# Optimization experiments

Hardware: AMD Instinct MI355X
Metric: run time of the kernel (lower is better)

Reference implementation:

```python
import jax, jax.numpy as jnp
import numpy as np

B, Himg, Wimg, C, HID, R = 16, 64, 64, 256, 512, 2
CLIP = 3.0
NULL_LOGIT = 0.0
WARMUP_ETA = 1.0


def _ln(x, g, b, eps=1e-5):
    m = x.mean(-1, keepdims=True)
    v = ((x - m) ** 2).mean(-1, keepdims=True)
    return (x - m) * jax.lax.rsqrt(v + eps) * g + b


def _mlp(x, W1, b1, W2, b2):
    # Linear -> GELU (erf, torch default) -> Linear
    return jax.nn.gelu(x @ W1 + b1, approximate=False) @ W2 + b2


def setup_inputs() -> dict:
    key = jax.random.key(0)
    ks = jax.random.split(key, 8)
    s = 0.02
    return {
        "states": jax.random.normal(ks[0], (B, Himg * Wimg, C), jnp.float32),
        "ln_c_g": jnp.ones((C,), jnp.float32),
        "ln_c_b": jnp.zeros((C,), jnp.float32),
        "parent_seed": jax.random.normal(ks[1], (1, 1, C), jnp.float32) * s,
        "dW1": jax.random.normal(ks[2], (3 * C, HID), jnp.float32) * s,
        "db1": jnp.zeros((HID,), jnp.float32),
        "dW2": jax.random.normal(ks[3], (HID, 1), jnp.float32) * s,
        "db2": jnp.zeros((1,), jnp.float32),
        "rW1": jax.random.normal(ks[4], (3 * C, HID), jnp.float32) * s,
        "rb1": jnp.zeros((HID,), jnp.float32),
        "rW2": jax.random.normal(ks[5], (HID, 1), jnp.float32) * s,
        "rb2": jnp.zeros((1,), jnp.float32),
        "vW": jax.random.normal(ks[6], (C, C), jnp.float32) * s,
        "vb": jnp.zeros((C,), jnp.float32),
        "e_bias": jnp.full((1,), -0.1, jnp.float32),
        "ln_o_g": jnp.ones((C,), jnp.float32),
        "ln_o_b": jnp.zeros((C,), jnp.float32),
        "image_h": Himg,
        "image_w": Wimg,
    }


def reference(states, ln_c_g, ln_c_b, parent_seed, dW1, db1, dW2, db2,
              rW1, rb1, rW2, rb2, vW, vb, e_bias, ln_o_g, ln_o_b,
              image_h, image_w):
    b = states.shape[0]
    ph, pw = image_h // R, image_w // R
    # [B,H,W,C] -> [B, ph*pw, R*R, C] local 2x2 child groups
    grid = states.reshape(b, image_h, image_w, C)
    groups = grid.reshape(b, ph, R, pw, R, C).transpose(0, 1, 3, 2, 4, 5)
    groups = groups.reshape(b, ph * pw, R * R, C)

    normalized = _ln(groups, ln_c_g, ln_c_b)            # child LayerNorm
    gm = normalized.mean(axis=2, keepdims=True)          # group mean (mask all-true)
    gm_b = jnp.broadcast_to(gm, normalized.shape)
    joint = jnp.concatenate([normalized, gm_b, normalized * gm_b], axis=-1)

    drive = _mlp(joint, dW1, db1, dW2, db2)              # [B,P,G,1]
    variance = ((normalized - gm) ** 2).mean(-1, keepdims=True)
    resistance = jax.nn.softplus(_mlp(joint, rW1, rb1, rW2, rb2)) + variance

    # EMLUnit: clipped drive/resistance energy with learned bias
    energy = jnp.clip(WARMUP_ETA * drive / (resistance + 1e-6) + e_bias,
                      -CLIP, CLIP)[..., 0]               # [B,P,G]

    # EMLResponsibility: null-aware softmax over children + null slot
    null = jnp.full(energy.shape[:-1] + (1,), NULL_LOGIT, energy.dtype)
    probs = jax.nn.softmax(jnp.concatenate([energy, null], axis=-1), axis=-1)
    weights = probs[..., :-1]                            # neighbor_weights [B,P,G]
    null_weight = probs[..., -1:]                        # [B,P,1]
    update_strength = 1.0 - null_weight                  # [B,P,1]

    values = normalized @ vW + vb                        # value_proj
    candidate = jnp.einsum('bpg,bpgc->bpc', weights, values)

    # EMLPrecisionUpdate with old_confidence=0: blend seed toward candidate
    old_state = parent_seed                              # broadcasts over [B,P,C]
    new_state = old_state + update_strength * (candidate - old_state)
    parent_state = _ln(new_state, ln_o_g, ln_o_b)
    return parent_state
```

## Files before the change

### kernel.cpp

```cpp
#include <hip/hip_runtime.h>
#include <hip/hip_bf16.h>
#include <math.h>

#define BATCH 16
#define PGRID 1024
#define NGRP  (BATCH*PGRID)
#define NELEM (NGRP*4)
#define CDIM  256
#define HID   512

#define OFF_NH    ((size_t)0)
#define OFF_NL    ((size_t)8388608)
#define OFF_GMH   ((size_t)16777216)
#define OFF_GML   ((size_t)18874368)
#define OFF_VAR   ((size_t)20971520)
#define OFF_DRIVE ((size_t)21037056)
#define OFF_RPRE  ((size_t)21102592)
#define OFF_WN    ((size_t)21168128)
#define OFF_US    ((size_t)25362432)
#define OFF_W1TH  ((size_t)25378816)
#define OFF_W1TL  ((size_t)25772032)

__device__ __forceinline__ unsigned short f2bf(float x) {
  unsigned u = __float_as_uint(x);
  unsigned r = u + 0x7FFFu + ((u >> 16) & 1u);
  return (unsigned short)(r >> 16);
}
__device__ __forceinline__ float bf2f(unsigned short h) {
  return __uint_as_float(((unsigned)h) << 16);
}

__device__ __forceinline__ void wave_reduce4(float v[4]) {
#pragma unroll
  for (int off = 1; off < 64; off <<= 1) {
#pragma unroll
    for (int i = 0; i < 4; ++i) v[i] += __shfl_xor(v[i], off, 64);
  }
}

__device__ __forceinline__ void block_reduce4(float v[4], float* sh ) {
  wave_reduce4(v);
  const int lane = threadIdx.x & 63, wid = threadIdx.x >> 6;
  __syncthreads();
  if (lane == 0) {
#pragma unroll
    for (int i = 0; i < 4; ++i) sh[wid * 4 + i] = v[i];
  }
  __syncthreads();
#pragma unroll
  for (int i = 0; i < 4; ++i) v[i] = sh[i] + sh[4 + i] + sh[8 + i] + sh[12 + i];
}

__global__ __launch_bounds__(256) void prep_kernel(
    const float* __restrict__ states,
    const float* __restrict__ ln_c_g, const float* __restrict__ ln_c_b,
    short* __restrict__ nh, short* __restrict__ nl,
    short* __restrict__ gmh, short* __restrict__ gml,
    float* __restrict__ varb, float* __restrict__ drive, float* __restrict__ rpre)
{
  __shared__ float sh[16];
  const int g = blockIdx.x;
  const int b = g >> 10;
  const int p = g & 1023;
  const int py = p >> 5, px = p & 31;
  const int c = threadIdx.x;

  float x[4];
#pragma unroll
  for (int s = 0; s < 4; ++s) {
    const int h = py * 2 + (s >> 1);
    const int w = px * 2 + (s & 1);
    x[s] = states[((size_t)(b * 4096 + h * 64 + w)) * CDIM + c];
  }

  float sum[4] = {x[0], x[1], x[2], x[3]};
  block_reduce4(sum, sh);
  float d[4];
#pragma unroll
  for (int s = 0; s < 4; ++s) d[s] = x[s] - sum[s] * (1.f / 256.f);

  float sq[4] = {d[0]*d[0], d[1]*d[1], d[2]*d[2], d[3]*d[3]};
  block_reduce4(sq, sh);

  const float gg = ln_c_g[c], bb = ln_c_b[c];
  float nn[4];
#pragma unroll
  for (int s = 0; s < 4; ++s)
    nn[s] = d[s] * rsqrtf(sq[s] * (1.f / 256.f) + 1e-5f) * gg + bb;

  const float gmc = 0.25f * (nn[0] + nn[1] + nn[2] + nn[3]);
  float e4[4];
#pragma unroll
  for (int s = 0; s < 4; ++s) { const float t = nn[s] - gmc; e4[s] = t * t; }
  block_reduce4(e4, sh);

  const size_t nb = (size_t)g * 4 * CDIM;
#pragma unroll
  for (int s = 0; s < 4; ++s) {
    const unsigned short h = f2bf(nn[s]);
    const unsigned short l = f2bf(nn[s] - bf2f(h));
    nh[nb + s * CDIM + c] = (short)h;
    nl[nb + s * CDIM + c] = (short)l;
  }
  {
    const unsigned short h = f2bf(gmc);
    const unsigned short l = f2bf(gmc - bf2f(h));
    gmh[(size_t)g * CDIM + c] = (short)h;
    gml[(size_t)g * CDIM + c] = (short)l;
  }
  if (c < 4) {
    varb[g * 4 + c] = e4[c] * (1.f / 256.f);
    drive[g * 4 + c] = 0.f;
    rpre[g * 4 + c] = 0.f;
  }
}

__global__ __launch_bounds__(256) void prew1_kernel(
    const float* __restrict__ dW1, const float* __restrict__ rW1,
    short* __restrict__ w1th, short* __restrict__ w1tl)
{
  const int col = blockIdx.x;
  const float* W1 = (col < 512) ? dW1 : rW1;
  const int cl = (col < 512) ? col : col - 512;
  for (int k = threadIdx.x; k < 768; k += 256) {
    const float x = W1[(size_t)k * HID + cl];
    const unsigned short h = f2bf(x);
    const unsigned short l = f2bf(x - bf2f(h));
    w1th[(size_t)col * 768 + k] = (short)h;
    w1tl[(size_t)col * 768 + k] = (short)l;
  }
}

typedef __attribute__((ext_vector_type(8))) short  frag_ab;
typedef __attribute__((ext_vector_type(4))) float  frag_cd;

#define AIDX(sec, row) ((sec) * 1024 + (row) * 8)

__global__ __launch_bounds__(256, 2) void mlp_gemm_mfma(
    const short* __restrict__ nh, const short* __restrict__ nl,
    const short* __restrict__ gmh, const short* __restrict__ gml,
    const short* __restrict__ w1th, const short* __restrict__ w1tl,
    const float* __restrict__ db1, const float* __restrict__ rb1,
    const float* __restrict__ dW2, const float* __restrict__ rW2,
    float* __restrict__ drive, float* __restrict__ rpre)
{
  __shared__ __align__(16) short Ah[8192];
  __shared__ __align__(16) short Al[8192];
  __shared__ __align__(16) short Bh[8192];
  __shared__ __align__(16) short Bl[8192];

  const int tid  = threadIdx.x;
  const int lane = tid & 63;
  const int w    = tid >> 6;
  const int wm   = w >> 1;
  const int wn   = w & 1;

  const int bid = blockIdx.x;
  const int xcd = bid & 7;
  const int lb  = bid >> 3;
  const int mt  = xcd * 64 + (lb >> 3);
  const int nt  = lb & 7;
  const int m_base = mt * 128;
  const int n_base = nt * 128;

  const int srow = tid & 127;
  const int sp   = tid >> 7;
  const int sp16 = sp * 16;
  const int sp2  = sp * 2;

  const short* nhrow = nh  + (size_t)(m_base + srow) * CDIM;
  const short* nlrow = nl  + (size_t)(m_base + srow) * CDIM;
  const short* ghrow = gmh + (size_t)((m_base + srow) >> 2) * CDIM;
  const short* glrow = gml + (size_t)((m_base + srow) >> 2) * CDIM;
  const short* bsrc_h = w1th + (size_t)(n_base + srow) * 768 + sp16;
  const short* bsrc_l = w1tl + (size_t)(n_base + srow) * 768 + sp16;

  frag_cd acc[4][4];
#pragma unroll
  for (int i = 0; i < 4; ++i)
#pragma unroll
    for (int j = 0; j < 4; ++j)
#pragma unroll
      for (int q = 0; q < 4; ++q) acc[i][j][q] = 0.f;

  frag_ab rA0, rA1, rA2, rA3, rA4, rA5, rA6, rA7;
  frag_ab sB0, sB1, sB2, sB3;

#define LOADA(K0) do {                                                   \
    const int k0_ = (K0);                                                \
    if (k0_ < 256) {                                                     \
      const short* p_ = nhrow + k0_ + sp16;                              \
      const short* q_ = nlrow + k0_ + sp16;                              \
      rA0 = *(const frag_ab*)(p_);  rA1 = *(const frag_ab*)(p_ + 8);     \
      rA2 = *(const frag_ab*)(q_);  rA3 = *(const frag_ab*)(q_ + 8);     \
    } else if (k0_ < 512) {                                              \
      const short* p_ = ghrow + (k0_ - 256) + sp16;                      \
      const short* q_ = glrow + (k0_ - 256) + sp16;                      \
      rA0 = *(const frag_ab*)(p_);  rA1 = *(const frag_ab*)(p_ + 8);     \
      rA2 = *(const frag_ab*)(q_);  rA3 = *(const frag_ab*)(q_ + 8);     \
    } else {                                                             \
      const int kb_ = k0_ - 512;                                         \
      const short* p_ = nhrow + kb_ + sp16;                              \
      const short* q_ = nlrow + kb_ + sp16;                              \
      const short* r_ = ghrow + kb_ + sp16;                              \
      const short* s_ = glrow + kb_ + sp16;                              \
      rA0 = *(const frag_ab*)(p_);  rA1 = *(const frag_ab*)(p_ + 8);     \
      rA2 = *(const frag_ab*)(q_);  rA3 = *(const frag_ab*)(q_ + 8);     \
      rA4 = *(const frag_ab*)(r_);  rA5 = *(const frag_ab*)(r_ + 8);     \
      rA6 = *(const frag_ab*)(s_);  rA7 = *(const frag_ab*)(s_ + 8);     \
    }                                                                    \
  } while (0)

#define LOADB(K0) do {                                                   \
    sB0 = *(const frag_ab*)(bsrc_h + (K0));                              \
    sB1 = *(const frag_ab*)(bsrc_h + (K0) + 8);                          \
    sB2 = *(const frag_ab*)(bsrc_l + (K0));                              \
    sB3 = *(const frag_ab*)(bsrc_l + (K0) + 8);                          \
  } while (0)

#define STOREAB(BUF, RAW) do {                                           \
    const int bo_ = (BUF) * 4096;                                        \
    if (RAW) {                                                           \
      *(frag_ab*)&Ah[bo_ + AIDX(sp2,     srow)] = rA0;                   \
      *(frag_ab*)&Ah[bo_ + AIDX(sp2 + 1, srow)] = rA1;                   \
      *(frag_ab*)&Al[bo_ + AIDX(sp2,     srow)] = rA2;                   \
      *(frag_ab*)&Al[bo_ + AIDX(sp2 + 1, srow)] = rA3;                   \
    } else {                                                             \
      frag_ab ph0, ph1, pl0, pl1;                                        \
      _Pragma("unroll")                                                  \
      for (int j_ = 0; j_ < 8; ++j_) {                                   \
        const float n0 = bf2f((unsigned short)rA0[j_]) + bf2f((unsigned short)rA2[j_]); \
        const float g0 = bf2f((unsigned short)rA4[j_]) + bf2f((unsigned short)rA6[j_]); \
        const float p0 = n0 * g0;                                        \
        const unsigned short h0_ = f2bf(p0);                             \
        ph0[j_] = (short)h0_; pl0[j_] = (short)f2bf(p0 - bf2f(h0_));     \
        const float n1 = bf2f((unsigned short)rA1[j_]) + bf2f((unsigned short)rA3[j_]); \
        const float g1 = bf2f((unsigned short)rA5[j_]) + bf2f((unsigned short)rA7[j_]); \
        const float p1 = n1 * g1;                                        \
        const unsigned short h1_ = f2bf(p1);                             \
        ph1[j_] = (short)h1_; pl1[j_] = (short)f2bf(p1 - bf2f(h1_));     \
      }                                                                  \
      *(frag_ab*)&Ah[bo_ + AIDX(sp2,     srow)] = ph0;                   \
      *(frag_ab*)&Ah[bo_ + AIDX(sp2 + 1, srow)] = ph1;                   \
      *(frag_ab*)&Al[bo_ + AIDX(sp2,     srow)] = pl0;                   \
      *(frag_ab*)&Al[bo_ + AIDX(sp2 + 1, srow)] = pl1;                   \
    }                                                                    \
    *(frag_ab*)&Bh[bo_ + AIDX(sp2,     srow)] = sB0;                     \
    *(frag_ab*)&Bh[bo_ + AIDX(sp2 + 1, srow)] = sB1;                     \
    *(frag_ab*)&Bl[bo_ + AIDX(sp2,     srow)] = sB2;                     \
    *(frag_ab*)&Bl[bo_ + AIDX(sp2 + 1, srow)] = sB3;                     \
  } while (0)

  LOADA(0); LOADB(0);
  STOREAB(0, true);
  __syncthreads();
  int cur = 0;

  const int l15 = lane & 15;
  const int sec = lane >> 4;

  for (int kk = 0; kk < 24; ++kk) {
    const bool havenext = (kk < 23);
    if (havenext) { const int k0 = (kk + 1) * 32; LOADA(k0); LOADB(k0); }

    const int bo = cur * 4096;
    frag_ab bhf[4], blf[4];
#pragma unroll
    for (int nf = 0; nf < 4; ++nf) {
      const int cb = bo + AIDX(sec, wn * 64 + nf * 16 + l15);
      bhf[nf] = *(const frag_ab*)&Bh[cb];
      blf[nf] = *(const frag_ab*)&Bl[cb];
    }
#pragma unroll
    for (int mf = 0; mf < 4; ++mf) {
      const int rb = bo + AIDX(sec, wm * 64 + mf * 16 + l15);
      const frag_ab ahf = *(const frag_ab*)&Ah[rb];
      const frag_ab alf = *(const frag_ab*)&Al[rb];
#pragma unroll
      for (int nf = 0; nf < 4; ++nf) {
        acc[mf][nf] = __builtin_amdgcn_mfma_f32_16x16x32_bf16(ahf, bhf[nf], acc[mf][nf], 0, 0, 0);
        acc[mf][nf] = __builtin_amdgcn_mfma_f32_16x16x32_bf16(ahf, blf[nf], acc[mf][nf], 0, 0, 0);
        acc[mf][nf] = __builtin_amdgcn_mfma_f32_16x16x32_bf16(alf, bhf[nf], acc[mf][nf], 0, 0, 0);
      }
    }

    if (havenext) {
      STOREAB(cur ^ 1, (kk + 1) < 16);
      __syncthreads();
      cur ^= 1;
    }
  }

  const bool is_d = (n_base < 512);
  const float* b1v = is_d ? db1 : rb1;
  const float* W2v = is_d ? dW2 : rW2;
  float* tgt = is_d ? drive : rpre;
  const int joff = n_base - (is_d ? 0 : 512) + wn * 64;

  float part[4][4];
#pragma unroll
  for (int i = 0; i < 4; ++i)
#pragma unroll
    for (int q = 0; q < 4; ++q) part[i][q] = 0.f;

#pragma unroll
  for (int nf = 0; nf < 4; ++nf) {
    const int j = joff + nf * 16 + l15;
    const float bb = b1v[j];
    const float ww = W2v[j];
#pragma unroll
    for (int mf = 0; mf < 4; ++mf)
#pragma unroll
      for (int q = 0; q < 4; ++q) {
        const float xv = acc[mf][nf][q] + bb;
        const float ge = 0.5f * xv * (1.f + erff(xv * 0.70710678118654752f));
        part[mf][q] = fmaf(ge, ww, part[mf][q]);
      }
  }
#pragma unroll
  for (int off = 1; off < 16; off <<= 1)
#pragma unroll
    for (int mf = 0; mf < 4; ++mf)
#pragma unroll
      for (int q = 0; q < 4; ++q)
        part[mf][q] += __shfl_xor(part[mf][q], off, 64);

  if (l15 == 0) {
    const int rq = lane >> 4;
#pragma unroll
    for (int mf = 0; mf < 4; ++mf)
#pragma unroll
      for (int q = 0; q < 4; ++q)
        atomicAdd(&tgt[m_base + wm * 64 + mf * 16 + rq * 4 + q], part[mf][q]);
  }
}

__global__ __launch_bounds__(256) void weights_kernel(
    const short* __restrict__ nh, const short* __restrict__ nl,
    const float* __restrict__ drive, const float* __restrict__ rpre,
    const float* __restrict__ varb,
    const float* __restrict__ db2, const float* __restrict__ rb2,
    const float* __restrict__ e_bias,
    float* __restrict__ wn, float* __restrict__ usb)
{
  const int g = blockIdx.x;
  const int c = threadIdx.x;
  const float eb = e_bias[0];
  const float b2d = db2[0], b2r = rb2[0];

  float w[4];
  float mx = 0.f;
#pragma unroll
  for (int s = 0; s < 4; ++s) {
    const float dr = drive[g * 4 + s] + b2d;
    const float rp = rpre[g * 4 + s] + b2r;
    const float va = varb[g * 4 + s];
    const float sp = fmaxf(rp, 0.f) + log1pf(expf(-fabsf(rp)));
    float en = dr / (sp + va + 1e-6f) + eb;
    en = fminf(3.f, fmaxf(-3.f, en));
    w[s] = en;
    mx = fmaxf(mx, en);
  }
  const float nullw = expf(-mx);
  float Z = nullw;
#pragma unroll
  for (int s = 0; s < 4; ++s) { w[s] = expf(w[s] - mx); Z += w[s]; }
  const float inv = 1.f / Z;

  float a = 0.f;
  const size_t nb = (size_t)g * 4 * CDIM;
#pragma unroll
  for (int s = 0; s < 4; ++s) {
    const size_t ix = nb + s * CDIM + c;
    const float nv = bf2f((unsigned short)nh[ix]) + bf2f((unsigned short)nl[ix]);
    a = fmaf(w[s] * inv, nv, a);
  }
  wn[(size_t)g * CDIM + c] = a;
  if (c == 0) usb[g] = 1.f - nullw * inv;
}

__global__ __launch_bounds__(256) void final_kernel(
    const float* __restrict__ wn, const float* __restrict__ usb,
    const float* __restrict__ vW, const float* __restrict__ vb,
    const float* __restrict__ seed,
    const float* __restrict__ ln_o_g, const float* __restrict__ ln_o_b,
    float* __restrict__ out)
{
  __shared__ float lwn[16][256];
  const int t = threadIdx.x;
  const int g0 = blockIdx.x * 16;
#pragma unroll
  for (int gi = 0; gi < 16; ++gi)
    lwn[gi][t] = wn[(size_t)(g0 + gi) * CDIM + t];
  __syncthreads();

  const int cq = (t & 63) * 4;
  const int gq = (t >> 6) * 4;

  float acc[4][4];
#pragma unroll
  for (int gi = 0; gi < 4; ++gi)
#pragma unroll
    for (int j = 0; j < 4; ++j) acc[gi][j] = 0.f;

  for (int k = 0; k < 256; ++k) {
    const float4 w4 = *(const float4*)(vW + (size_t)k * CDIM + cq);
#pragma unroll
    for (int gi = 0; gi < 4; ++gi) {
      const float a = lwn[gq + gi][k];
      acc[gi][0] = fmaf(a, w4.x, acc[gi][0]);
      acc[gi][1] = fmaf(a, w4.y, acc[gi][1]);
      acc[gi][2] = fmaf(a, w4.z, acc[gi][2]);
      acc[gi][3] = fmaf(a, w4.w, acc[gi][3]);
    }
  }

  const float4 sd  = *(const float4*)(seed + cq);
  const float4 og  = *(const float4*)(ln_o_g + cq);
  const float4 ob  = *(const float4*)(ln_o_b + cq);
  const float4 vb4 = *(const float4*)(vb + cq);

#pragma unroll
  for (int gi = 0; gi < 4; ++gi) {
    const float us = usb[g0 + gq + gi];
    float nv[4];
    nv[0] = sd.x + us * (acc[gi][0] + us * vb4.x - sd.x);
    nv[1] = sd.y + us * (acc[gi][1] + us * vb4.y - sd.y);
    nv[2] = sd.z + us * (acc[gi][2] + us * vb4.z - sd.z);
    nv[3] = sd.w + us * (acc[gi][3] + us * vb4.w - sd.w);

    float s = nv[0] + nv[1] + nv[2] + nv[3];
#pragma unroll
    for (int off = 1; off < 64; off <<= 1) s += __shfl_xor(s, off, 64);
    const float m = s * (1.f / 256.f);

    const float d0 = nv[0] - m, d1 = nv[1] - m, d2 = nv[2] - m, d3 = nv[3] - m;
    float q = d0 * d0 + d1 * d1 + d2 * d2 + d3 * d3;
#pragma unroll
    for (int off = 1; off < 64; off <<= 1) q += __shfl_xor(q, off, 64);
    const float rstd = rsqrtf(q * (1.f / 256.f) + 1e-5f);

    float4 o;
    o.x = d0 * rstd * og.x + ob.x;
    o.y = d1 * rstd * og.y + ob.y;
    o.z = d2 * rstd * og.z + ob.z;
    o.w = d3 * rstd * og.w + ob.w;
    *(float4*)(out + (size_t)(g0 + gq + gi) * CDIM + cq) = o;
  }
}

extern "C" void kernel_launch(void* const* d_in, const int* in_sizes, int n_in,
                              void* d_out, int out_size, void* d_ws, size_t ws_size,
                              hipStream_t stream)
{
  const float* states = (const float*)d_in[0];
  const float* ln_c_g = (const float*)d_in[1];
  const float* ln_c_b = (const float*)d_in[2];
  const float* seed   = (const float*)d_in[3];
  const float* dW1    = (const float*)d_in[4];
  const float* db1    = (const float*)d_in[5];
  const float* dW2    = (const float*)d_in[6];
  const float* db2    = (const float*)d_in[7];
  const float* rW1    = (const float*)d_in[8];
  const float* rb1    = (const float*)d_in[9];
  const float* rW2    = (const float*)d_in[10];
  const float* rb2    = (const float*)d_in[11];
  const float* vW     = (const float*)d_in[12];
  const float* vb     = (const float*)d_in[13];
  const float* e_bias = (const float*)d_in[14];
  const float* ln_o_g = (const float*)d_in[15];
  const float* ln_o_b = (const float*)d_in[16];
  float* out = (float*)d_out;

  float* ws    = (float*)d_ws;
  short* nhb   = (short*)(ws + OFF_NH);
  short* nlb   = (short*)(ws + OFF_NL);
  short* gmhb  = (short*)(ws + OFF_GMH);
  short* gmlb  = (short*)(ws + OFF_GML);
  float* varb  = ws + OFF_VAR;
  float* drive = ws + OFF_DRIVE;
  float* rpre  = ws + OFF_RPRE;
  float* wnb   = ws + OFF_WN;
  float* usb   = ws + OFF_US;
  short* w1th  = (short*)(ws + OFF_W1TH);
  short* w1tl  = (short*)(ws + OFF_W1TL);

  prep_kernel<<<NGRP, 256, 0, stream>>>(states, ln_c_g, ln_c_b,
                                        nhb, nlb, gmhb, gmlb, varb, drive, rpre);

  prew1_kernel<<<1024, 256, 0, stream>>>(dW1, rW1, w1th, w1tl);

  mlp_gemm_mfma<<<4096, 256, 0, stream>>>(nhb, nlb, gmhb, gmlb, w1th, w1tl,
                                          db1, rb1, dW2, rW2, drive, rpre);

  weights_kernel<<<NGRP, 256, 0, stream>>>(nhb, nlb, drive, rpre, varb,
                                           db2, rb2, e_bias, wnb, usb);

  final_kernel<<<NGRP / 16, 256, 0, stream>>>(wnb, usb, vW, vb, seed,
                                              ln_o_g, ln_o_b, out);
}
```

Baseline: 722.3 us.

## Stage GEMM tiles via direct global-to-LDS loads with single buffer

Replaces the register-staged, double-buffered LDS tile loads in the MLP GEMM with global_load_lds direct-to-LDS copies into a single buffer, halving shared memory. The launch-bounds occupancy hint rises from 2 to 4 blocks per CU. Register pressure and LDS footprint drop, which should allow more resident waves to hide latency. The cost is that global loads no longer overlap the MFMA compute within a block: each iteration now syncs, issues loads, and syncs again.

```diff
diff --git a/kernel.cpp b/kernel.cpp
--- a/kernel.cpp
+++ b/kernel.cpp
@@ -30,6 +30,12 @@
   return __uint_as_float(((unsigned)h) << 16);
 }
 
+__device__ __forceinline__ void gld16(const short* g, short* l) {
+  __builtin_amdgcn_global_load_lds(
+      (const __attribute__((address_space(1))) void*)g,
+      (__attribute__((address_space(3))) void*)l, 16, 0, 0);
+}
+
 __device__ __forceinline__ void wave_reduce4(float v[4]) {
 #pragma unroll
   for (int off = 1; off < 64; off <<= 1) {
@@ -136,7 +142,7 @@
 
 #define AIDX(sec, row) ((sec) * 1024 + (row) * 8)
 
-__global__ __launch_bounds__(256, 2) void mlp_gemm_mfma(
+__global__ __launch_bounds__(256, 4) void mlp_gemm_mfma(
     const short* __restrict__ nh, const short* __restrict__ nl,
     const short* __restrict__ gmh, const short* __restrict__ gml,
     const short* __restrict__ w1th, const short* __restrict__ w1tl,
@@ -144,10 +150,10 @@
     const float* __restrict__ dW2, const float* __restrict__ rW2,
     float* __restrict__ drive, float* __restrict__ rpre)
 {
-  __shared__ __align__(16) short Ah[8192];
-  __shared__ __align__(16) short Al[8192];
-  __shared__ __align__(16) short Bh[8192];
-  __shared__ __align__(16) short Bl[8192];
+  __shared__ __align__(16) short Ah[4096];
+  __shared__ __align__(16) short Al[4096];
+  __shared__ __align__(16) short Bh[4096];
+  __shared__ __align__(16) short Bl[4096];
 
   const int tid  = threadIdx.x;
   const int lane = tid & 63;
@@ -184,96 +190,78 @@
       for (int q = 0; q < 4; ++q) acc[i][j][q] = 0.f;
 
   frag_ab rA0, rA1, rA2, rA3, rA4, rA5, rA6, rA7;
-  frag_ab sB0, sB1, sB2, sB3;
-
-#define LOADA(K0) do {                                                   \
-    const int k0_ = (K0);                                                \
-    if (k0_ < 256) {                                                     \
-      const short* p_ = nhrow + k0_ + sp16;                              \
-      const short* q_ = nlrow + k0_ + sp16;                              \
-      rA0 = *(const frag_ab*)(p_);  rA1 = *(const frag_ab*)(p_ + 8);     \
-      rA2 = *(const frag_ab*)(q_);  rA3 = *(const frag_ab*)(q_ + 8);     \
-    } else if (k0_ < 512) {                                              \
-      const short* p_ = ghrow + (k0_ - 256) + sp16;                      \
-      const short* q_ = glrow + (k0_ - 256) + sp16;                      \
-      rA0 = *(const frag_ab*)(p_);  rA1 = *(const frag_ab*)(p_ + 8);     \
-      rA2 = *(const frag_ab*)(q_);  rA3 = *(const frag_ab*)(q_ + 8);     \
-    } else {                                                             \
-      const int kb_ = k0_ - 512;                                         \
-      const short* p_ = nhrow + kb_ + sp16;                              \
-      const short* q_ = nlrow + kb_ + sp16;                              \
-      const short* r_ = ghrow + kb_ + sp16;                              \
-      const short* s_ = glrow + kb_ + sp16;                              \
-      rA0 = *(const frag_ab*)(p_);  rA1 = *(const frag_ab*)(p_ + 8);     \
-      rA2 = *(const frag_ab*)(q_);  rA3 = *(const frag_ab*)(q_ + 8);     \
-      rA4 = *(const frag_ab*)(r_);  rA5 = *(const frag_ab*)(r_ + 8);     \
-      rA6 = *(const frag_ab*)(s_);  rA7 = *(const frag_ab*)(s_ + 8);     \
+
+#define STAGE_B(K0) do {                                                 \
+    gld16(bsrc_h + (K0),     &Bh[AIDX(sp2,     srow)]);                  \
+    gld16(bsrc_h + (K0) + 8, &Bh[AIDX(sp2 + 1, srow)]);                  \
+    gld16(bsrc_l + (K0),     &Bl[AIDX(sp2,     srow)]);                  \
+    gld16(bsrc_l + (K0) + 8, &Bl[AIDX(sp2 + 1, srow)]);                  \
+  } while (0)
+
+#define STAGE_A_RAW(K0) do {                                             \
+    const short* ph_ = ((K0) < 256 ? nhrow + (K0)                        \
+                                   : ghrow + ((K0) - 256)) + sp16;       \
+    const short* pl_ = ((K0) < 256 ? nlrow + (K0)                        \
+                                   : glrow + ((K0) - 256)) + sp16;       \
+    gld16(ph_,     &Ah[AIDX(sp2,     srow)]);                            \
+    gld16(ph_ + 8, &Ah[AIDX(sp2 + 1, srow)]);                            \
+    gld16(pl_,     &Al[AIDX(sp2,     srow)]);                            \
+    gld16(pl_ + 8, &Al[AIDX(sp2 + 1, srow)]);                            \
+  } while (0)
+
+#define LOADA2(K0) do {                                                  \
+    const int kb_ = (K0) - 512;                                          \
+    const short* p_ = nhrow + kb_ + sp16;                                \
+    const short* q_ = nlrow + kb_ + sp16;                                \
+    const short* r_ = ghrow + kb_ + sp16;                                \
+    const short* s_ = glrow + kb_ + sp16;                                \
+    rA0 = *(const frag_ab*)(p_);  rA1 = *(const frag_ab*)(p_ + 8);       \
+    rA2 = *(const frag_ab*)(q_);  rA3 = *(const frag_ab*)(q_ + 8);       \
+    rA4 = *(const frag_ab*)(r_);  rA5 = *(const frag_ab*)(r_ + 8);       \
+    rA6 = *(const frag_ab*)(s_);  rA7 = *(const frag_ab*)(s_ + 8);       \
+  } while (0)
+
+#define CONVSTORE_A() do {                                               \
+    frag_ab ph0, ph1, pl0, pl1;                                          \
+    _Pragma("unroll")                                                    \
+    for (int j_ = 0; j_ < 8; ++j_) {                                     \
+      const float n0 = bf2f((unsigned short)rA0[j_]) + bf2f((unsigned short)rA2[j_]); \
+      const float g0 = bf2f((unsigned short)rA4[j_]) + bf2f((unsigned short)rA6[j_]); \
+      const float p0 = n0 * g0;                                          \
+      const unsigned short h0_ = f2bf(p0);                               \
+      ph0[j_] = (short)h0_; pl0[j_] = (short)f2bf(p0 - bf2f(h0_));       \
+      const float n1 = bf2f((unsigned short)rA1[j_]) + bf2f((unsigned short)rA3[j_]); \
+      const float g1 = bf2f((unsigned short)rA5[j_]) + bf2f((unsigned short)rA7[j_]); \
+      const float p1 = n1 * g1;                                          \
+      const unsigned short h1_ = f2bf(p1);                               \
+      ph1[j_] = (short)h1_; pl1[j_] = (short)f2bf(p1 - bf2f(h1_));       \
     }                                                                    \
+    *(frag_ab*)&Ah[AIDX(sp2,     srow)] = ph0;                           \
+    *(frag_ab*)&Ah[AIDX(sp2 + 1, srow)] = ph1;                           \
+    *(frag_ab*)&Al[AIDX(sp2,     srow)] = pl0;                           \
+    *(frag_ab*)&Al[AIDX(sp2 + 1, srow)] = pl1;                           \
   } while (0)
 
-#define LOADB(K0) do {                                                   \
-    sB0 = *(const frag_ab*)(bsrc_h + (K0));                              \
-    sB1 = *(const frag_ab*)(bsrc_h + (K0) + 8);                          \
-    sB2 = *(const frag_ab*)(bsrc_l + (K0));                              \
-    sB3 = *(const frag_ab*)(bsrc_l + (K0) + 8);                          \
-  } while (0)
-
-#define STOREAB(BUF, RAW) do {                                           \
-    const int bo_ = (BUF) * 4096;                                        \
-    if (RAW) {                                                           \
-      *(frag_ab*)&Ah[bo_ + AIDX(sp2,     srow)] = rA0;                   \
-      *(frag_ab*)&Ah[bo_ + AIDX(sp2 + 1, srow)] = rA1;                   \
-      *(frag_ab*)&Al[bo_ + AIDX(sp2,     srow)] = rA2;                   \
-      *(frag_ab*)&Al[bo_ + AIDX(sp2 + 1, srow)] = rA3;                   \
-    } else {                                                             \
-      frag_ab ph0, ph1, pl0, pl1;                                        \
-      _Pragma("unroll")                                                  \
-      for (int j_ = 0; j_ < 8; ++j_) {                                   \
-        const float n0 = bf2f((unsigned short)rA0[j_]) + bf2f((unsigned short)rA2[j_]); \
-        const float g0 = bf2f((unsigned short)rA4[j_]) + bf2f((unsigned short)rA6[j_]); \
-        const float p0 = n0 * g0;                                        \
-        const unsigned short h0_ = f2bf(p0);                             \
-        ph0[j_] = (short)h0_; pl0[j_] = (short)f2bf(p0 - bf2f(h0_));     \
-        const float n1 = bf2f((unsigned short)rA1[j_]) + bf2f((unsigned short)rA3[j_]); \
-        const float g1 = bf2f((unsigned short)rA5[j_]) + bf2f((unsigned short)rA7[j_]); \
-        const float p1 = n1 * g1;                                        \
-        const unsigned short h1_ = f2bf(p1);                             \
-        ph1[j_] = (short)h1_; pl1[j_] = (short)f2bf(p1 - bf2f(h1_));     \
-      }                                                                  \
-      *(frag_ab*)&Ah[bo_ + AIDX(sp2,     srow)] = ph0;                   \
-      *(frag_ab*)&Ah[bo_ + AIDX(sp2 + 1, srow)] = ph1;                   \
-      *(frag_ab*)&Al[bo_ + AIDX(sp2,     srow)] = pl0;                   \
-      *(frag_ab*)&Al[bo_ + AIDX(sp2 + 1, srow)] = pl1;                   \
-    }                                                                    \
-    *(frag_ab*)&Bh[bo_ + AIDX(sp2,     srow)] = sB0;                     \
-    *(frag_ab*)&Bh[bo_ + AIDX(sp2 + 1, srow)] = sB1;                     \
-    *(frag_ab*)&Bl[bo_ + AIDX(sp2,     srow)] = sB2;                     \
-    *(frag_ab*)&Bl[bo_ + AIDX(sp2 + 1, srow)] = sB3;                     \
-  } while (0)
-
-  LOADA(0); LOADB(0);
-  STOREAB(0, true);
+  STAGE_B(0);
+  STAGE_A_RAW(0);
   __syncthreads();
-  int cur = 0;
 
   const int l15 = lane & 15;
   const int sec = lane >> 4;
 
   for (int kk = 0; kk < 24; ++kk) {
-    const bool havenext = (kk < 23);
-    if (havenext) { const int k0 = (kk + 1) * 32; LOADA(k0); LOADB(k0); }
-
-    const int bo = cur * 4096;
+    if (kk >= 15 && kk < 23) { LOADA2((kk + 1) * 32); }
+
     frag_ab bhf[4], blf[4];
 #pragma unroll
     for (int nf = 0; nf < 4; ++nf) {
-      const int cb = bo + AIDX(sec, wn * 64 + nf * 16 + l15);
+      const int cb = AIDX(sec, wn * 64 + nf * 16 + l15);
       bhf[nf] = *(const frag_ab*)&Bh[cb];
       blf[nf] = *(const frag_ab*)&Bl[cb];
     }
 #pragma unroll
     for (int mf = 0; mf < 4; ++mf) {
-      const int rb = bo + AIDX(sec, wm * 64 + mf * 16 + l15);
+      const int rb = AIDX(sec, wm * 64 + mf * 16 + l15);
       const frag_ab ahf = *(const frag_ab*)&Ah[rb];
       const frag_ab alf = *(const frag_ab*)&Al[rb];
 #pragma unroll
@@ -284,10 +272,13 @@
       }
     }
 
-    if (havenext) {
-      STOREAB(cur ^ 1, (kk + 1) < 16);
+    if (kk < 23) {
       __syncthreads();
-      cur ^= 1;
+      const int k0 = (kk + 1) * 32;
+      STAGE_B(k0);
+      if (k0 < 512) STAGE_A_RAW(k0);
+      else          CONVSTORE_A();
+      __syncthreads();
     }
   }
 
```

Measured after the change: 1.267 ms. 75.4% more time.
